# Kernel tuning notes

Hardware: AMD Instinct MI355X
Metric: run time of the kernel (lower is better)

Reference implementation:

```python
import jax, jax.numpy as jnp
import numpy as np

B, R, D, H = 8192, 6, 1024, 256
TEMP = 0.5
SINKHORN_ITERS = 5


def rmsnorm(x, g, eps=1e-6):
    return x * jax.lax.rsqrt(jnp.mean(x * x, axis=-1, keepdims=True) + eps) * g


def setup_inputs() -> dict:
    key = jax.random.key(0)
    ks = jax.random.split(key, 24)
    def p(k, shape, fan):
        return jax.random.normal(k, shape, jnp.float32) / np.float32(np.sqrt(fan))
    return {
        'source_roles': jax.random.normal(ks[0], (B, R, D), jnp.float32),
        'target_roles': jax.random.normal(ks[1], (B, R, D), jnp.float32),
        # role_encoder: Linear(D,H) -> RMSNorm(H) -> SwiGLU(H, 2H) -> Linear(H,H)
        'W1': p(ks[2], (H, D), D), 'b1': jnp.zeros((H,), jnp.float32),
        'g1': jnp.ones((H,), jnp.float32),
        'Wa': p(ks[3], (2 * H, H), H),  # SwiGLU gate proj
        'Wb': p(ks[4], (2 * H, H), H),  # SwiGLU value proj
        'Wc': p(ks[5], (H, 2 * H), 2 * H),  # SwiGLU down proj
        'W2': p(ks[6], (H, H), H), 'b2': jnp.zeros((H,), jnp.float32),
        # map_score: Bilinear(H, H, 1)
        'Wbil': p(ks[7], (H, H), H), 'bbil': jnp.zeros((1,), jnp.float32),
        # answer_proj: Linear(2H,2H) -> GELU -> Linear(2H,D) -> RMSNorm(D)
        'Wa1': p(ks[8], (2 * H, 2 * H), 2 * H), 'ba1': jnp.zeros((2 * H,), jnp.float32),
        'Wa2': p(ks[9], (D, 2 * H), 2 * H), 'ba2': jnp.zeros((D,), jnp.float32),
        'g2': jnp.ones((D,), jnp.float32),
        # confidence_head: Linear(1,1) -> Sigmoid (input is a scalar statistic per batch)
        'Wc1': p(ks[10], (1, 1), 1), 'bc1': jnp.zeros((1,), jnp.float32),
    }


def reference(source_roles, target_roles, W1, b1, g1, Wa, Wb, Wc, W2, b2,
              Wbil, bbil, Wa1, ba1, Wa2, ba2, g2, Wc1, bc1):
    def role_encoder(x):  # [B,R,D] -> [B,R,H]
        x = x @ W1.T + b1
        x = rmsnorm(x, g1)
        x = (jax.nn.silu(x @ Wa.T) * (x @ Wb.T)) @ Wc.T  # SwiGLU
        return x @ W2.T + b2

    src_enc = role_encoder(source_roles)  # [B,R,H]
    tgt_enc = role_encoder(target_roles)  # [B,R,H]

    # Bilinear pairwise score: [B, R_src, R_tgt]
    log_alpha = (jnp.einsum('bih,hk,bjk->bij', src_enc, Wbil, tgt_enc) + bbil) / TEMP

    def sinkhorn_step(la, _):
        la = la - jax.nn.logsumexp(la, axis=-1, keepdims=True)
        la = la - jax.nn.logsumexp(la, axis=-2, keepdims=True)
        return la, None

    log_alpha, _ = jax.lax.scan(sinkhorn_step, log_alpha, None, length=SINKHORN_ITERS)
    mapping = jnp.exp(log_alpha)  # doubly-stochastic [B,R,R]

    mapped_src = jnp.einsum('bij,bjh->bih', mapping, tgt_enc)  # [B,R,H]

    diff = jnp.mean(jnp.abs(mapped_src - src_enc), axis=-1, keepdims=True)  # [B,R,1]
    conf_in = jnp.mean(diff, axis=-2)  # [B,1]
    confidence = jax.nn.sigmoid(conf_in @ Wc1.T + bc1).squeeze(-1)  # [B]

    combined = jnp.concatenate([mapped_src, tgt_enc], axis=-1)  # [B,R,2H]
    a = jax.nn.gelu(combined @ Wa1.T + ba1)
    answer = rmsnorm(a @ Wa2.T + ba2, g2)  # [B,R,D]
    return answer, mapping, mapped_src, confidence
```

## Files before the change

### kernel.cpp

```cpp
#include <hip/hip_runtime.h>
#include <hip/hip_bf16.h>


typedef float f32x4 __attribute__((ext_vector_type(4)));
typedef short s16x8 __attribute__((ext_vector_type(8)));
typedef short s16x4 __attribute__((ext_vector_type(4)));

__device__ __forceinline__ unsigned short f2bf(float x) {
  unsigned int u = __float_as_uint(x);
  u += 0x7FFFu + ((u >> 16) & 1u);
  return (unsigned short)(u >> 16);
}
__device__ __forceinline__ float bf2f(unsigned short b) {
  return __uint_as_float(((unsigned int)b) << 16);
}

template<bool SPLIT, int ACT>
__global__ __launch_bounds__(256, 2)
void gemm_nt(const float* __restrict__ A,
             const short* __restrict__ Whi, const short* __restrict__ Wlo,
             const float* __restrict__ bias, float* __restrict__ C,
             int K, int N)
{
  constexpr int BM = 128, BN = 128, BK = 64;
  __shared__ __attribute__((aligned(16))) short sAhi[BM * BK];
  __shared__ __attribute__((aligned(16))) short sBhi[BN * BK];
  __shared__ __attribute__((aligned(16))) short sAlo[SPLIT ? BM * BK : 8];
  __shared__ __attribute__((aligned(16))) short sBlo[SPLIT ? BN * BK : 8];

  const int tid = threadIdx.x;
  const int n0 = blockIdx.x * BN;
  const int m0 = blockIdx.y * BM;
  const int lane = tid & 63, w = tid >> 6;
  const int wr = (w >> 1) * 64, wc = (w & 1) * 64;

  f32x4 acc[4][4] = {};

  for (int k0 = 0; k0 < K; k0 += BK) {
    __syncthreads();
#pragma unroll
    for (int it = 0; it < 8; ++it) {
      int f = it * 256 + tid;
      int r = f >> 4, q = f & 15;
      f32x4 v = *reinterpret_cast<const f32x4*>(A + (size_t)(m0 + r) * K + k0 + q * 4);
      s16x4 hi, lo;
#pragma unroll
      for (int j = 0; j < 4; ++j) {
        unsigned short h = f2bf(v[j]);
        hi[j] = (short)h;
        if (SPLIT) lo[j] = (short)f2bf(v[j] - bf2f(h));
      }
      int off = r * 64 + (((q >> 1) ^ (r & 7)) << 3) + ((q & 1) << 2);
      *reinterpret_cast<s16x4*>(&sAhi[off]) = hi;
      if (SPLIT) *reinterpret_cast<s16x4*>(&sAlo[off]) = lo;
    }
#pragma unroll
    for (int it = 0; it < 4; ++it) {
      int c = it * 256 + tid;
      int r = c >> 3, ch = c & 7;
      size_t g = (size_t)(n0 + r) * K + k0 + ch * 8;
      int off = r * 64 + ((ch ^ (r & 7)) << 3);
      *reinterpret_cast<s16x8*>(&sBhi[off]) = *reinterpret_cast<const s16x8*>(Whi + g);
      if (SPLIT) *reinterpret_cast<s16x8*>(&sBlo[off]) = *reinterpret_cast<const s16x8*>(Wlo + g);
    }
    __syncthreads();
#pragma unroll
    for (int kc = 0; kc < 2; ++kc) {
      s16x8 ah[4], al[4];
#pragma unroll
      for (int mt = 0; mt < 4; ++mt) {
        int r = wr + mt * 16 + (lane & 15);
        int off = r * 64 + ((((kc << 2) + (lane >> 4)) ^ (r & 7)) << 3);
        ah[mt] = *reinterpret_cast<const s16x8*>(&sAhi[off]);
        if (SPLIT) al[mt] = *reinterpret_cast<const s16x8*>(&sAlo[off]);
      }
#pragma unroll
      for (int nt = 0; nt < 4; ++nt) {
        int r = wc + nt * 16 + (lane & 15);
        int off = r * 64 + ((((kc << 2) + (lane >> 4)) ^ (r & 7)) << 3);
        s16x8 bh = *reinterpret_cast<const s16x8*>(&sBhi[off]);
        s16x8 bl = {};
        if (SPLIT) bl = *reinterpret_cast<const s16x8*>(&sBlo[off]);
#pragma unroll
        for (int mt = 0; mt < 4; ++mt) {
          acc[mt][nt] = __builtin_amdgcn_mfma_f32_16x16x32_bf16(ah[mt], bh, acc[mt][nt], 0, 0, 0);
          if (SPLIT) {
            acc[mt][nt] = __builtin_amdgcn_mfma_f32_16x16x32_bf16(ah[mt], bl, acc[mt][nt], 0, 0, 0);
            acc[mt][nt] = __builtin_amdgcn_mfma_f32_16x16x32_bf16(al[mt], bh, acc[mt][nt], 0, 0, 0);
          }
        }
      }
    }
  }
#pragma unroll
  for (int mt = 0; mt < 4; ++mt) {
#pragma unroll
    for (int nt = 0; nt < 4; ++nt) {
      int cc = n0 + wc + nt * 16 + (lane & 15);
      float bv = bias ? bias[cc] : 0.f;
#pragma unroll
      for (int j = 0; j < 4; ++j) {
        int rr = m0 + wr + mt * 16 + (lane >> 4) * 4 + j;
        float v = acc[mt][nt][j] + bv;
        if (ACT == 1) {
          float x3 = v * v * v;
          v = 0.5f * v * (1.f + tanhf(0.7978845608028654f * (v + 0.044715f * x3)));
        }
        C[(size_t)rr * N + cc] = v;
      }
    }
  }
}

__global__ __launch_bounds__(256)
void prep_w(const float* __restrict__ W1, const float* __restrict__ Wa,
            const float* __restrict__ Wb, const float* __restrict__ Wc,
            const float* __restrict__ W2, const float* __restrict__ Wbil,
            const float* __restrict__ Wa1, const float* __restrict__ Wa2,
            short* __restrict__ hi, short* __restrict__ lo)
{
  int e0 = (blockIdx.x * 256 + threadIdx.x) * 4;
  const float* src; int local; bool tr = false;
  if      (e0 < 262144)  { src = W1;   local = e0; }
  else if (e0 < 393216)  { src = Wa;   local = e0 - 262144; }
  else if (e0 < 524288)  { src = Wb;   local = e0 - 393216; }
  else if (e0 < 655360)  { src = Wc;   local = e0 - 524288; }
  else if (e0 < 720896)  { src = W2;   local = e0 - 655360; }
  else if (e0 < 786432)  { src = Wbil; local = e0 - 720896; tr = true; }
  else if (e0 < 1048576) { src = Wa1;  local = e0 - 786432; }
  else                   { src = Wa2;  local = e0 - 1048576; }
  float v[4];
  if (tr) {
#pragma unroll
    for (int t = 0; t < 4; ++t) {
      int li = local + t;
      int n = li >> 8, hh = li & 255;
      v[t] = src[hh * 256 + n];
    }
  } else {
    f32x4 tv = *reinterpret_cast<const f32x4*>(src + local);
    v[0] = tv[0]; v[1] = tv[1]; v[2] = tv[2]; v[3] = tv[3];
  }
#pragma unroll
  for (int t = 0; t < 4; ++t) {
    unsigned short h = f2bf(v[t]);
    hi[e0 + t] = (short)h;
    lo[e0 + t] = (short)f2bf(v[t] - bf2f(h));
  }
}

template<int L>
__global__ __launch_bounds__(256)
void rmsnorm_k(float* __restrict__ x, const float* __restrict__ g)
{
  constexpr int NV = L / 256;
  int wid = threadIdx.x >> 6, lane = threadIdx.x & 63;
  size_t row = (size_t)blockIdx.x * 4 + wid;
  float* p = x + row * L;
  f32x4 v[NV];
  float ss = 0.f;
#pragma unroll
  for (int i = 0; i < NV; ++i) {
    v[i] = *reinterpret_cast<const f32x4*>(p + (i * 64 + lane) * 4);
    ss += v[i][0] * v[i][0] + v[i][1] * v[i][1] + v[i][2] * v[i][2] + v[i][3] * v[i][3];
  }
#pragma unroll
  for (int o = 32; o > 0; o >>= 1) ss += __shfl_xor(ss, o);
  float s = rsqrtf(ss * (1.f / L) + 1e-6f);
#pragma unroll
  for (int i = 0; i < NV; ++i) {
    f32x4 gg = *reinterpret_cast<const f32x4*>(g + (i * 64 + lane) * 4);
    f32x4 o4;
#pragma unroll
    for (int j = 0; j < 4; ++j) o4[j] = v[i][j] * s * gg[j];
    *reinterpret_cast<f32x4*>(p + (i * 64 + lane) * 4) = o4;
  }
}

__global__ __launch_bounds__(256)
void silu_mul_k(float* __restrict__ t1, const float* __restrict__ t2)
{
  size_t i = (size_t)blockIdx.x * 256 + threadIdx.x;
  f32x4 a = reinterpret_cast<f32x4*>(t1)[i];
  f32x4 b = reinterpret_cast<const f32x4*>(t2)[i];
  f32x4 o;
#pragma unroll
  for (int j = 0; j < 4; ++j) {
    float x = a[j];
    o[j] = (x / (1.f + expf(-x))) * b[j];
  }
  reinterpret_cast<f32x4*>(t1)[i] = o;
}

__global__ __launch_bounds__(256)
void concat_k(const float* __restrict__ msrc, const float* __restrict__ tenc,
              float* __restrict__ comb)
{
  size_t i = (size_t)blockIdx.x * 256 + threadIdx.x;
  size_t r = i >> 7; int q = (int)(i & 127);
  f32x4 v;
  if (q < 64) v = reinterpret_cast<const f32x4*>(msrc)[r * 64 + q];
  else        v = reinterpret_cast<const f32x4*>(tenc)[r * 64 + (q - 64)];
  reinterpret_cast<f32x4*>(comb)[i] = v;
}

__global__ __launch_bounds__(64)
void sinkhorn_k(const float* __restrict__ P, const float* __restrict__ Se,
                const float* __restrict__ Te, const float* __restrict__ bbil,
                const float* __restrict__ Wc1, const float* __restrict__ bc1,
                float* __restrict__ omap, float* __restrict__ omapped,
                float* __restrict__ oconf)
{
  int b = blockIdx.x, lane = threadIdx.x;
  __shared__ __attribute__((aligned(16))) float sP[6 * 260];
  __shared__ __attribute__((aligned(16))) float sT[6 * 260];
  __shared__ __attribute__((aligned(16))) float sS[6 * 260];
  const f32x4* gp = reinterpret_cast<const f32x4*>(P + (size_t)b * 1536);
  const f32x4* gt = reinterpret_cast<const f32x4*>(Te + (size_t)b * 1536);
  const f32x4* gs = reinterpret_cast<const f32x4*>(Se + (size_t)b * 1536);
#pragma unroll
  for (int i0 = 0; i0 < 6; ++i0) {
    int i = i0 * 64 + lane;
    int r = i >> 6, c = i & 63;
    *reinterpret_cast<f32x4*>(&sP[r * 260 + c * 4]) = gp[i];
    *reinterpret_cast<f32x4*>(&sT[r * 260 + c * 4]) = gt[i];
    *reinterpret_cast<f32x4*>(&sS[r * 260 + c * 4]) = gs[i];
  }
  __syncthreads();
  int i = lane / 6, j = lane - i * 6;
  float la = 0.f;
  if (lane < 36) {
    const float* pr = &sP[i * 260];
    const float* tr = &sT[j * 260];
    float d = 0.f;
    for (int k = 0; k < 256; ++k) d = fmaf(pr[k], tr[k], d);
    la = (d + bbil[0]) * 2.0f;
  }
#pragma unroll
  for (int it = 0; it < 5; ++it) {
    float m = -1e30f, s = 0.f;
#pragma unroll
    for (int t = 0; t < 6; ++t) m = fmaxf(m, __shfl(la, i * 6 + t));
#pragma unroll
    for (int t = 0; t < 6; ++t) s += expf(__shfl(la, i * 6 + t) - m);
    la -= m + logf(s);
    m = -1e30f; s = 0.f;
#pragma unroll
    for (int t = 0; t < 6; ++t) m = fmaxf(m, __shfl(la, t * 6 + j));
#pragma unroll
    for (int t = 0; t < 6; ++t) s += expf(__shfl(la, t * 6 + j) - m);
    la -= m + logf(s);
  }
  float mp = (lane < 36) ? expf(la) : 0.f;
  if (lane < 36) omap[(size_t)b * 36 + lane] = mp;
  float mm[36];
#pragma unroll
  for (int t = 0; t < 36; ++t) mm[t] = __shfl(mp, t);
  float asum = 0.f;
#pragma unroll
  for (int ii = 0; ii < 6; ++ii) {
    f32x4 av = {0.f, 0.f, 0.f, 0.f};
#pragma unroll
    for (int k = 0; k < 6; ++k) {
      f32x4 tv = *reinterpret_cast<const f32x4*>(&sT[k * 260 + lane * 4]);
      av += tv * mm[ii * 6 + k];
    }
    f32x4 sv = *reinterpret_cast<const f32x4*>(&sS[ii * 260 + lane * 4]);
    *reinterpret_cast<f32x4*>(omapped + (size_t)b * 1536 + ii * 256 + lane * 4) = av;
    asum += fabsf(av[0] - sv[0]) + fabsf(av[1] - sv[1]) +
            fabsf(av[2] - sv[2]) + fabsf(av[3] - sv[3]);
  }
#pragma unroll
  for (int o = 32; o > 0; o >>= 1) asum += __shfl_xor(asum, o);
  if (lane == 0) {
    float ci = asum * (1.f / 1536.f);
    float z = ci * Wc1[0] + bc1[0];
    oconf[b] = 1.f / (1.f + expf(-z));
  }
}

extern "C" void kernel_launch(void* const* d_in, const int* in_sizes, int n_in,
                              void* d_out, int out_size, void* d_ws, size_t ws_size,
                              hipStream_t stream)
{
  const float* src_roles = (const float*)d_in[0];
  const float* tgt_roles = (const float*)d_in[1];
  const float* W1   = (const float*)d_in[2];
  const float* b1   = (const float*)d_in[3];
  const float* g1   = (const float*)d_in[4];
  const float* Wa   = (const float*)d_in[5];
  const float* Wb   = (const float*)d_in[6];
  const float* Wc   = (const float*)d_in[7];
  const float* W2   = (const float*)d_in[8];
  const float* b2   = (const float*)d_in[9];
  const float* Wbil = (const float*)d_in[10];
  const float* bbil = (const float*)d_in[11];
  const float* Wa1  = (const float*)d_in[12];
  const float* ba1  = (const float*)d_in[13];
  const float* Wa2  = (const float*)d_in[14];
  const float* ba2  = (const float*)d_in[15];
  const float* g2   = (const float*)d_in[16];
  const float* Wc1  = (const float*)d_in[17];
  const float* bc1  = (const float*)d_in[18];

  float* out = (float*)d_out;
  float* o_answer  = out;
  float* o_mapping = out + 50331648;
  float* o_mapped  = out + 50626560;
  float* o_conf    = out + 63209472;
  float* t1   = out;
  float* encS = out + 25165824;
  float* encT = out + 37748736;

  float* h  = (float*)d_ws;
  float* t2 = (float*)d_ws + 12582912;
  short* whi = (short*)((float*)d_ws + 37748736);
  short* wlo = whi + 1572864;

  const int oW1 = 0, oWa = 262144, oWb = 393216, oWc = 524288, oW2 = 655360,
            oWbt = 720896, oWa1 = 786432, oWa2 = 1048576;

  hipLaunchKernelGGL(prep_w, dim3(1536), dim3(256), 0, stream,
                     W1, Wa, Wb, Wc, W2, Wbil, Wa1, Wa2, whi, wlo);

  for (int s = 0; s < 2; ++s) {
    const float* X = (s == 0) ? src_roles : tgt_roles;
    float* enc = (s == 0) ? encS : encT;
    hipLaunchKernelGGL((gemm_nt<true, 0>), dim3(2, 384), dim3(256), 0, stream,
                       X, whi + oW1, wlo + oW1, b1, h, 1024, 256);
    hipLaunchKernelGGL((rmsnorm_k<256>), dim3(12288), dim3(256), 0, stream, h, g1);
    hipLaunchKernelGGL((gemm_nt<true, 0>), dim3(4, 384), dim3(256), 0, stream,
                       h, whi + oWa, wlo + oWa, (const float*)nullptr, t1, 256, 512);
    hipLaunchKernelGGL((gemm_nt<true, 0>), dim3(4, 384), dim3(256), 0, stream,
                       h, whi + oWb, wlo + oWb, (const float*)nullptr, t2, 256, 512);
    hipLaunchKernelGGL(silu_mul_k, dim3(24576), dim3(256), 0, stream, t1, t2);
    hipLaunchKernelGGL((gemm_nt<true, 0>), dim3(2, 384), dim3(256), 0, stream,
                       t1, whi + oWc, wlo + oWc, (const float*)nullptr, h, 512, 256);
    hipLaunchKernelGGL((gemm_nt<true, 0>), dim3(2, 384), dim3(256), 0, stream,
                       h, whi + oW2, wlo + oW2, b2, enc, 256, 256);
  }
  hipLaunchKernelGGL((gemm_nt<true, 0>), dim3(2, 384), dim3(256), 0, stream,
                     encS, whi + oWbt, wlo + oWbt, (const float*)nullptr, t2, 256, 256);
  hipLaunchKernelGGL(sinkhorn_k, dim3(8192), dim3(64), 0, stream,
                     t2, encS, encT, bbil, Wc1, bc1, o_mapping, o_mapped, o_conf);
  hipLaunchKernelGGL(concat_k, dim3(24576), dim3(256), 0, stream, o_mapped, encT, t1);
  hipLaunchKernelGGL((gemm_nt<false, 1>), dim3(4, 384), dim3(256), 0, stream,
                     t1, whi + oWa1, wlo + oWa1, ba1, t2, 512, 512);
  hipLaunchKernelGGL((gemm_nt<false, 0>), dim3(8, 384), dim3(256), 0, stream,
                     t2, whi + oWa2, wlo + oWa2, ba2, o_answer, 512, 1024);
  hipLaunchKernelGGL((rmsnorm_k<1024>), dim3(12288), dim3(256), 0, stream, o_answer, g2);
}
```

Before: 1.572 ms.

## Store intermediates as bf16 hi/lo planes and fuse silu-mul and concat into GEMMs

Intermediate activations are now written by each GEMM epilogue as pre-split bf16 hi/lo planes, so later GEMMs load them directly instead of reading fp32 and converting in the A-load loop. SiLU-multiply is fused into the Wb GEMM epilogue, and the concat kernel is replaced by a two-source A load in the Wa1 GEMM. The GELU output is stored as bf16 only. Together these remove two kernels and reduce activation traffic, at the cost of a more complex templated GEMM and a larger workspace.

Result: faster. 1.436 ms (-8.6%).

```diff
diff --git a/kernel.cpp b/kernel.cpp
--- a/kernel.cpp
+++ b/kernel.cpp
@@ -15,12 +15,20 @@
   return __uint_as_float(((unsigned int)b) << 16);
 }
 
-template<bool SPLIT, int ACT>
+enum { A_F32 = 0, A_PLANES = 1, A_BF16 = 2, A_CAT = 3 };
+enum { E_NONE = 0, E_GELU = 1, E_SILUMUL = 2 };
+enum { O_F32 = 0, O_PLANES = 1, O_BF16 = 2 };
+
+template<int AIN, bool SPLIT, int EPI, int OUT>
 __global__ __launch_bounds__(256, 2)
-void gemm_nt(const float* __restrict__ A,
-             const short* __restrict__ Whi, const short* __restrict__ Wlo,
-             const float* __restrict__ bias, float* __restrict__ C,
-             int K, int N)
+void gemm2(const float* __restrict__ Af,
+           const short* __restrict__ Ahi, const short* __restrict__ Alo,
+           const short* __restrict__ Acat2,
+           const short* __restrict__ Whi, const short* __restrict__ Wlo,
+           const float* __restrict__ bias,
+           float* __restrict__ Cf, short* __restrict__ Chi, short* __restrict__ Clo,
+           const short* __restrict__ Xhi, const short* __restrict__ Xlo,
+           int K, int N)
 {
   constexpr int BM = 128, BN = 128, BK = 64;
   __shared__ __attribute__((aligned(16))) short sAhi[BM * BK];
@@ -38,21 +46,42 @@
 
   for (int k0 = 0; k0 < K; k0 += BK) {
     __syncthreads();
-#pragma unroll
-    for (int it = 0; it < 8; ++it) {
-      int f = it * 256 + tid;
-      int r = f >> 4, q = f & 15;
-      f32x4 v = *reinterpret_cast<const f32x4*>(A + (size_t)(m0 + r) * K + k0 + q * 4);
-      s16x4 hi, lo;
-#pragma unroll
-      for (int j = 0; j < 4; ++j) {
-        unsigned short h = f2bf(v[j]);
-        hi[j] = (short)h;
-        if (SPLIT) lo[j] = (short)f2bf(v[j] - bf2f(h));
+    if (AIN == A_F32) {
+#pragma unroll
+      for (int it = 0; it < 8; ++it) {
+        int f = it * 256 + tid;
+        int r = f >> 4, q = f & 15;
+        f32x4 v = *reinterpret_cast<const f32x4*>(Af + (size_t)(m0 + r) * K + k0 + q * 4);
+        s16x4 hi, lo;
+#pragma unroll
+        for (int j = 0; j < 4; ++j) {
+          unsigned short h = f2bf(v[j]);
+          hi[j] = (short)h;
+          if (SPLIT) lo[j] = (short)f2bf(v[j] - bf2f(h));
+        }
+        int off = r * 64 + (((q >> 1) ^ (r & 7)) << 3) + ((q & 1) << 2);
+        *reinterpret_cast<s16x4*>(&sAhi[off]) = hi;
+        if (SPLIT) *reinterpret_cast<s16x4*>(&sAlo[off]) = lo;
       }
-      int off = r * 64 + (((q >> 1) ^ (r & 7)) << 3) + ((q & 1) << 2);
-      *reinterpret_cast<s16x4*>(&sAhi[off]) = hi;
-      if (SPLIT) *reinterpret_cast<s16x4*>(&sAlo[off]) = lo;
+    } else {
+#pragma unroll
+      for (int it = 0; it < 4; ++it) {
+        int c = it * 256 + tid;
+        int r = c >> 3, ch = c & 7;
+        int off = r * 64 + ((ch ^ (r & 7)) << 3);
+        const short* srcHi = nullptr; const short* srcLo = nullptr;
+        if (AIN == A_PLANES || AIN == A_BF16) {
+          size_t g = (size_t)(m0 + r) * K + k0 + ch * 8;
+          srcHi = Ahi + g;
+          if (SPLIT) srcLo = Alo + g;
+        } else {
+          int kk = k0 + ch * 8;
+          srcHi = (kk < 256) ? (Ahi + (size_t)(m0 + r) * 256 + kk)
+                             : (Acat2 + (size_t)(m0 + r) * 256 + (kk - 256));
+        }
+        *reinterpret_cast<s16x8*>(&sAhi[off]) = *reinterpret_cast<const s16x8*>(srcHi);
+        if (SPLIT) *reinterpret_cast<s16x8*>(&sAlo[off]) = *reinterpret_cast<const s16x8*>(srcLo);
+      }
     }
 #pragma unroll
     for (int it = 0; it < 4; ++it) {
@@ -102,11 +131,23 @@
       for (int j = 0; j < 4; ++j) {
         int rr = m0 + wr + mt * 16 + (lane >> 4) * 4 + j;
         float v = acc[mt][nt][j] + bv;
-        if (ACT == 1) {
+        size_t idx = (size_t)rr * N + cc;
+        if (EPI == E_GELU) {
           float x3 = v * v * v;
           v = 0.5f * v * (1.f + tanhf(0.7978845608028654f * (v + 0.044715f * x3)));
+        } else if (EPI == E_SILUMUL) {
+          float xa = bf2f((unsigned short)Xhi[idx]) + bf2f((unsigned short)Xlo[idx]);
+          v *= xa / (1.f + expf(-xa));
         }
-        C[(size_t)rr * N + cc] = v;
+        if (OUT == O_F32) {
+          Cf[idx] = v;
+        } else if (OUT == O_BF16) {
+          Chi[idx] = (short)f2bf(v);
+        } else {
+          unsigned short hh = f2bf(v);
+          Chi[idx] = (short)hh;
+          Clo[idx] = (short)f2bf(v - bf2f(hh));
+        }
       }
     }
   }
@@ -149,14 +190,44 @@
   }
 }
 
-template<int L>
 __global__ __launch_bounds__(256)
-void rmsnorm_k(float* __restrict__ x, const float* __restrict__ g)
-{
-  constexpr int NV = L / 256;
+void rmsnorm_planes256(short* __restrict__ xhi, short* __restrict__ xlo,
+                       const float* __restrict__ g)
+{
   int wid = threadIdx.x >> 6, lane = threadIdx.x & 63;
   size_t row = (size_t)blockIdx.x * 4 + wid;
-  float* p = x + row * L;
+  short* ph = xhi + row * 256 + lane * 4;
+  short* pl = xlo + row * 256 + lane * 4;
+  s16x4 h4 = *reinterpret_cast<const s16x4*>(ph);
+  s16x4 l4 = *reinterpret_cast<const s16x4*>(pl);
+  float v[4]; float ss = 0.f;
+#pragma unroll
+  for (int j = 0; j < 4; ++j) {
+    v[j] = bf2f((unsigned short)h4[j]) + bf2f((unsigned short)l4[j]);
+    ss += v[j] * v[j];
+  }
+#pragma unroll
+  for (int o = 32; o > 0; o >>= 1) ss += __shfl_xor(ss, o);
+  float s = rsqrtf(ss * (1.f / 256.f) + 1e-6f);
+  f32x4 gg = *reinterpret_cast<const f32x4*>(g + lane * 4);
+#pragma unroll
+  for (int j = 0; j < 4; ++j) {
+    float o = v[j] * s * gg[j];
+    unsigned short hh = f2bf(o);
+    h4[j] = (short)hh;
+    l4[j] = (short)f2bf(o - bf2f(hh));
+  }
+  *reinterpret_cast<s16x4*>(ph) = h4;
+  *reinterpret_cast<s16x4*>(pl) = l4;
+}
+
+__global__ __launch_bounds__(256)
+void rmsnorm_f32_1024(float* __restrict__ x, const float* __restrict__ g)
+{
+  constexpr int NV = 4;
+  int wid = threadIdx.x >> 6, lane = threadIdx.x & 63;
+  size_t row = (size_t)blockIdx.x * 4 + wid;
+  float* p = x + row * 1024;
   f32x4 v[NV];
   float ss = 0.f;
 #pragma unroll
@@ -166,7 +237,7 @@
   }
 #pragma unroll
   for (int o = 32; o > 0; o >>= 1) ss += __shfl_xor(ss, o);
-  float s = rsqrtf(ss * (1.f / L) + 1e-6f);
+  float s = rsqrtf(ss * (1.f / 1024.f) + 1e-6f);
 #pragma unroll
   for (int i = 0; i < NV; ++i) {
     f32x4 gg = *reinterpret_cast<const f32x4*>(g + (i * 64 + lane) * 4);
@@ -177,54 +248,35 @@
   }
 }
 
-__global__ __launch_bounds__(256)
-void silu_mul_k(float* __restrict__ t1, const float* __restrict__ t2)
-{
-  size_t i = (size_t)blockIdx.x * 256 + threadIdx.x;
-  f32x4 a = reinterpret_cast<f32x4*>(t1)[i];
-  f32x4 b = reinterpret_cast<const f32x4*>(t2)[i];
-  f32x4 o;
-#pragma unroll
-  for (int j = 0; j < 4; ++j) {
-    float x = a[j];
-    o[j] = (x / (1.f + expf(-x))) * b[j];
-  }
-  reinterpret_cast<f32x4*>(t1)[i] = o;
-}
-
-__global__ __launch_bounds__(256)
-void concat_k(const float* __restrict__ msrc, const float* __restrict__ tenc,
-              float* __restrict__ comb)
-{
-  size_t i = (size_t)blockIdx.x * 256 + threadIdx.x;
-  size_t r = i >> 7; int q = (int)(i & 127);
-  f32x4 v;
-  if (q < 64) v = reinterpret_cast<const f32x4*>(msrc)[r * 64 + q];
-  else        v = reinterpret_cast<const f32x4*>(tenc)[r * 64 + (q - 64)];
-  reinterpret_cast<f32x4*>(comb)[i] = v;
-}
-
 __global__ __launch_bounds__(64)
-void sinkhorn_k(const float* __restrict__ P, const float* __restrict__ Se,
-                const float* __restrict__ Te, const float* __restrict__ bbil,
+void sinkhorn_k(const float* __restrict__ P,
+                const short* __restrict__ Sehi, const short* __restrict__ Selo,
+                const short* __restrict__ Tehi, const short* __restrict__ Telo,
+                const float* __restrict__ bbil,
                 const float* __restrict__ Wc1, const float* __restrict__ bc1,
                 float* __restrict__ omap, float* __restrict__ omapped,
-                float* __restrict__ oconf)
+                short* __restrict__ omappedb, float* __restrict__ oconf)
 {
   int b = blockIdx.x, lane = threadIdx.x;
   __shared__ __attribute__((aligned(16))) float sP[6 * 260];
   __shared__ __attribute__((aligned(16))) float sT[6 * 260];
   __shared__ __attribute__((aligned(16))) float sS[6 * 260];
   const f32x4* gp = reinterpret_cast<const f32x4*>(P + (size_t)b * 1536);
-  const f32x4* gt = reinterpret_cast<const f32x4*>(Te + (size_t)b * 1536);
-  const f32x4* gs = reinterpret_cast<const f32x4*>(Se + (size_t)b * 1536);
 #pragma unroll
   for (int i0 = 0; i0 < 6; ++i0) {
     int i = i0 * 64 + lane;
     int r = i >> 6, c = i & 63;
     *reinterpret_cast<f32x4*>(&sP[r * 260 + c * 4]) = gp[i];
-    *reinterpret_cast<f32x4*>(&sT[r * 260 + c * 4]) = gt[i];
-    *reinterpret_cast<f32x4*>(&sS[r * 260 + c * 4]) = gs[i];
+    size_t e = (size_t)b * 1536 + i * 4;
+    s16x4 th = *reinterpret_cast<const s16x4*>(Tehi + e);
+    s16x4 tl = *reinterpret_cast<const s16x4*>(Telo + e);
+    s16x4 sh = *reinterpret_cast<const s16x4*>(Sehi + e);
+    s16x4 sl = *reinterpret_cast<const s16x4*>(Selo + e);
+#pragma unroll
+    for (int j = 0; j < 4; ++j) {
+      sT[r * 260 + c * 4 + j] = bf2f((unsigned short)th[j]) + bf2f((unsigned short)tl[j]);
+      sS[r * 260 + c * 4 + j] = bf2f((unsigned short)sh[j]) + bf2f((unsigned short)sl[j]);
+    }
   }
   __syncthreads();
   int i = lane / 6, j = lane - i * 6;
@@ -266,7 +318,12 @@
       av += tv * mm[ii * 6 + k];
     }
     f32x4 sv = *reinterpret_cast<const f32x4*>(&sS[ii * 260 + lane * 4]);
-    *reinterpret_cast<f32x4*>(omapped + (size_t)b * 1536 + ii * 256 + lane * 4) = av;
+    size_t e = (size_t)b * 1536 + ii * 256 + lane * 4;
+    *reinterpret_cast<f32x4*>(omapped + e) = av;
+    s16x4 mb;
+#pragma unroll
+    for (int jj = 0; jj < 4; ++jj) mb[jj] = (short)f2bf(av[jj]);
+    *reinterpret_cast<s16x4*>(omappedb + e) = mb;
     asum += fabsf(av[0] - sv[0]) + fabsf(av[1] - sv[1]) +
             fabsf(av[2] - sv[2]) + fabsf(av[3] - sv[3]);
   }
@@ -308,45 +365,58 @@
   float* o_mapping = out + 50331648;
   float* o_mapped  = out + 50626560;
   float* o_conf    = out + 63209472;
-  float* t1   = out;
-  float* encS = out + 25165824;
-  float* encT = out + 37748736;
-
-  float* h  = (float*)d_ws;
-  float* t2 = (float*)d_ws + 12582912;
-  short* whi = (short*)((float*)d_ws + 37748736);
-  short* wlo = whi + 1572864;
+  short* xa_hi = (short*)out;
+  short* xa_lo = xa_hi + 25165824;
+  short* t_hi  = xa_lo + 25165824;
+  short* t_lo  = t_hi + 25165824;
+
+  float* P = (float*)d_ws;
+  short* sb = (short*)((float*)d_ws + 12582912);
+  short* whi  = sb;
+  short* wlo  = whi + 1572864;
+  short* h_hi = wlo + 1572864;
+  short* h_lo = h_hi + 12582912;
+  short* u_hi = h_lo + 12582912;
+  short* u_lo = u_hi + 12582912;
+  short* eS_hi = u_lo + 12582912;
+  short* eS_lo = eS_hi + 12582912;
+  short* eT_hi = eS_lo + 12582912;
+  short* eT_lo = eT_hi + 12582912;
+  short* act   = eT_lo + 12582912;
+  short* mapb  = act + 25165824;
 
   const int oW1 = 0, oWa = 262144, oWb = 393216, oWc = 524288, oW2 = 655360,
             oWbt = 720896, oWa1 = 786432, oWa2 = 1048576;
+  const short* NS = nullptr; const float* NF = nullptr;
+  float* NFo = nullptr; short* NSo = nullptr;
 
   hipLaunchKernelGGL(prep_w, dim3(1536), dim3(256), 0, stream,
                      W1, Wa, Wb, Wc, W2, Wbil, Wa1, Wa2, whi, wlo);
 
   for (int s = 0; s < 2; ++s) {
     const float* X = (s == 0) ? src_roles : tgt_roles;
-    float* enc = (s == 0) ? encS : encT;
-    hipLaunchKernelGGL((gemm_nt<true, 0>), dim3(2, 384), dim3(256), 0, stream,
-                       X, whi + oW1, wlo + oW1, b1, h, 1024, 256);
-    hipLaunchKernelGGL((rmsnorm_k<256>), dim3(12288), dim3(256), 0, stream, h, g1);
-    hipLaunchKernelGGL((gemm_nt<true, 0>), dim3(4, 384), dim3(256), 0, stream,
-                       h, whi + oWa, wlo + oWa, (const float*)nullptr, t1, 256, 512);
-    hipLaunchKernelGGL((gemm_nt<true, 0>), dim3(4, 384), dim3(256), 0, stream,
-                       h, whi + oWb, wlo + oWb, (const float*)nullptr, t2, 256, 512);
-    hipLaunchKernelGGL(silu_mul_k, dim3(24576), dim3(256), 0, stream, t1, t2);
-    hipLaunchKernelGGL((gemm_nt<true, 0>), dim3(2, 384), dim3(256), 0, stream,
-                       t1, whi + oWc, wlo + oWc, (const float*)nullptr, h, 512, 256);
-    hipLaunchKernelGGL((gemm_nt<true, 0>), dim3(2, 384), dim3(256), 0, stream,
-                       h, whi + oW2, wlo + oW2, b2, enc, 256, 256);
-  }
-  hipLaunchKernelGGL((gemm_nt<true, 0>), dim3(2, 384), dim3(256), 0, stream,
-                     encS, whi + oWbt, wlo + oWbt, (const float*)nullptr, t2, 256, 256);
+    short* e_hi = (s == 0) ? eS_hi : eT_hi;
+    short* e_lo = (s == 0) ? eS_lo : eT_lo;
+    hipLaunchKernelGGL((gemm2<A_F32, true, E_NONE, O_PLANES>), dim3(2, 384), dim3(256), 0, stream,
+                       X, NS, NS, NS, whi + oW1, wlo + oW1, b1, NFo, h_hi, h_lo, NS, NS, 1024, 256);
+    hipLaunchKernelGGL(rmsnorm_planes256, dim3(12288), dim3(256), 0, stream, h_hi, h_lo, g1);
+    hipLaunchKernelGGL((gemm2<A_PLANES, true, E_NONE, O_PLANES>), dim3(4, 384), dim3(256), 0, stream,
+                       NF, h_hi, h_lo, NS, whi + oWa, wlo + oWa, NF, NFo, xa_hi, xa_lo, NS, NS, 256, 512);
+    hipLaunchKernelGGL((gemm2<A_PLANES, true, E_SILUMUL, O_PLANES>), dim3(4, 384), dim3(256), 0, stream,
+                       NF, h_hi, h_lo, NS, whi + oWb, wlo + oWb, NF, NFo, t_hi, t_lo, xa_hi, xa_lo, 256, 512);
+    hipLaunchKernelGGL((gemm2<A_PLANES, true, E_NONE, O_PLANES>), dim3(2, 384), dim3(256), 0, stream,
+                       NF, t_hi, t_lo, NS, whi + oWc, wlo + oWc, NF, NFo, u_hi, u_lo, NS, NS, 512, 256);
+    hipLaunchKernelGGL((gemm2<A_PLANES, true, E_NONE, O_PLANES>), dim3(2, 384), dim3(256), 0, stream,
+                       NF, u_hi, u_lo, NS, whi + oW2, wlo + oW2, b2, NFo, e_hi, e_lo, NS, NS, 256, 256);
+  }
+  hipLaunchKernelGGL((gemm2<A_PLANES, true, E_NONE, O_F32>), dim3(2, 384), dim3(256), 0, stream,
+                     NF, eS_hi, eS_lo, NS, whi + oWbt, wlo + oWbt, NF, P, NSo, NSo, NS, NS, 256, 256);
   hipLaunchKernelGGL(sinkhorn_k, dim3(8192), dim3(64), 0, stream,
-                     t2, encS, encT, bbil, Wc1, bc1, o_mapping, o_mapped, o_conf);
-  hipLaunchKernelGGL(concat_k, dim3(24576), dim3(256), 0, stream, o_mapped, encT, t1);
-  hipLaunchKernelGGL((gemm_nt<false, 1>), dim3(4, 384), dim3(256), 0, stream,
-                     t1, whi + oWa1, wlo + oWa1, ba1, t2, 512, 512);
-  hipLaunchKernelGGL((gemm_nt<false, 0>), dim3(8, 384), dim3(256), 0, stream,
-                     t2, whi + oWa2, wlo + oWa2, ba2, o_answer, 512, 1024);
-  hipLaunchKernelGGL((rmsnorm_k<1024>), dim3(12288), dim3(256), 0, stream, o_answer, g2);
-}
+                     P, eS_hi, eS_lo, eT_hi, eT_lo, bbil, Wc1, bc1,
+                     o_mapping, o_mapped, mapb, o_conf);
+  hipLaunchKernelGGL((gemm2<A_CAT, false, E_GELU, O_BF16>), dim3(4, 384), dim3(256), 0, stream,
+                     NF, mapb, NS, eT_hi, whi + oWa1, wlo + oWa1, ba1, NFo, act, NSo, NS, NS, 512, 512);
+  hipLaunchKernelGGL((gemm2<A_BF16, false, E_NONE, O_F32>), dim3(8, 384), dim3(256), 0, stream,
+                     NF, act, NS, NS, whi + oWa2, wlo + oWa2, ba2, o_answer, NSo, NSo, NS, NS, 512, 1024);
+  hipLaunchKernelGGL(rmsnorm_f32_1024, dim3(12288), dim3(256), 0, stream, o_answer, g2);
+}
```
